# Kernel tuning notes

Measured on AMD Instinct MI355X. Metric: run time of the kernel, lower is better.

Reference implementation:

```python
import jax, jax.numpy as jnp
import numpy as np
import math

D = 256
N = 2048
B = 8
N_PLUS_1 = 2048  # masked index (1-based) in the score matrix


def setup_inputs() -> dict:
    key = jax.random.key(0)
    k1, k2, k3, k4, k5 = jax.random.split(key, 5)
    scale = 1.0 / math.sqrt(D)
    return {
        "Z_in": jax.random.normal(k1, (B, D + 1, N), dtype=jnp.float32),
        "A_l": jax.random.normal(k2, (D, D), dtype=jnp.float32) * scale,
        "r_l": jax.random.normal(k3, (1,), dtype=jnp.float32),
        "B_l": jax.random.normal(k4, (D, D), dtype=jnp.float32) * scale,
        "C_l": jax.random.normal(k5, (D, D), dtype=jnp.float32) * scale,
    }


def reference(Z_in, A_l, r_l, B_l, C_l):
    # Z_in: (B, d+1, N)
    X = Z_in[:, :D, :]   # (B, d, N)
    Y = Z_in[:, D:, :]   # (B, 1, N)
    U = jnp.einsum('ij,bjn->bin', B_l, X)  # (B, d, N)
    W = jnp.einsum('ij,bjn->bin', C_l, X)  # (B, d, N)
    scores = jnp.einsum('bdn,bdm->bnm', U, W)  # (B, N, N) = U^T W
    att = jax.nn.relu(scores)                  # h_type == 'relu'
    # zero the (n_plus_1-1, n_plus_1-1) diagonal entry of the attention core
    att = att.at[:, N_PLUS_1 - 1, N_PLUS_1 - 1].set(0.0)
    X_att = jnp.einsum('bdn,bnm->bdm', X, att)  # (B, d, N)
    X_out = X + jnp.einsum('ij,bjm->bim', A_l, X_att)
    Y_out = Y + r_l * jnp.einsum('bdn,bnm->bdm', Y, att)
    return jnp.concatenate([X_out, Y_out], axis=1)  # (B, d+1, N)
```

## Files before the change

kernel.cpp:

```cpp
#include <hip/hip_runtime.h>

#define D 256
#define N 2048
#define NB 8
#define ZSTRIDE (257 * 2048)

typedef __attribute__((ext_vector_type(8))) short short8;
typedef __attribute__((ext_vector_type(4))) short short4v;
typedef __attribute__((ext_vector_type(4))) float f32x4;

#define MFMA(a, b, c) __builtin_amdgcn_mfma_f32_16x16x32_bf16((a), (b), (c), 0, 0, 0)

#define GLOAD_LDS16(g, s) __builtin_amdgcn_global_load_lds( \
    (const __attribute__((address_space(1))) void*)(g),     \
    (__attribute__((address_space(3))) void*)(s), 16, 0, 0)

#define VMCNT(Nstr) asm volatile("s_waitcnt vmcnt(" Nstr ")" ::: "memory")
#define BAR() __builtin_amdgcn_s_barrier()

__device__ __forceinline__ short f2bf(float f) {
    unsigned u = __builtin_bit_cast(unsigned, f);
    u += 0x7fffu + ((u >> 16) & 1u);
    return (short)(u >> 16);
}
__device__ __forceinline__ float bf2f(short s) {
    unsigned u = ((unsigned)(unsigned short)s) << 16;
    return __builtin_bit_cast(float, u);
}

__global__ __launch_bounds__(256) void front_kernel(
    const float* __restrict__ B_l, const float* __restrict__ C_l,
    const float* __restrict__ A_l, const float* __restrict__ Z,
    short* __restrict__ G, short* __restrict__ Ab, short* __restrict__ Yb,
    float* __restrict__ accY, short* __restrict__ Xt, int zeroAcc)
{
    typedef __attribute__((ext_vector_type(4))) float f4;
    __shared__ short t[64][68];
    int blk = blockIdx.x, tid = threadIdx.x;
    if (blk < 352) {
        if (blk < 256) {
            float s = 0.f;
            #pragma unroll 8
            for (int k = 0; k < 256; ++k)
                s += B_l[k * 256 + blk] * C_l[k * 256 + tid];
            G[blk * 256 + tid] = f2bf(s);
        } else if (blk < 320) {
            int base = (blk - 256) * 1024 + tid;
            #pragma unroll
            for (int r = 0; r < 4; ++r) {
                int idx = base + r * 256;
                Ab[idx] = f2bf(A_l[idx]);
            }
        } else if (blk < 336) {
            int base = (blk - 320) * 1024 + tid;
            #pragma unroll
            for (int r = 0; r < 4; ++r) {
                int idx = base + r * 256;
                int b = idx >> 11, n = idx & 2047;
                Yb[idx] = f2bf(Z[(size_t)b * ZSTRIDE + 256 * N + n]);
            }
        } else if (zeroAcc) {
            int i = (blk - 336) * 256 + tid;
            f32x4 z = {0.f, 0.f, 0.f, 0.f};
            *(f32x4*)(accY + (size_t)i * 4) = z;
        }
        return;
    }
    int tblk = blk - 352;
    int b = tblk & 7;
    int dt = (tblk >> 3) & 3;
    int nt = tblk >> 5;
    int d0 = dt * 64, n0 = nt * 64;
    const float* ZB = Z + (size_t)b * ZSTRIDE;
    #pragma unroll
    for (int k = 0; k < 4; ++k) {
        int f = tid + k * 256;
        int r = f >> 4, c4 = f & 15;
        f4 v = *(const f4*)(ZB + (size_t)(d0 + r) * N + n0 + c4 * 4);
        #pragma unroll
        for (int j = 0; j < 4; ++j) t[r][c4 * 4 + j] = f2bf(v[j]);
    }
    __syncthreads();
    short* XtB = Xt + (size_t)b * (N * D);
    #pragma unroll
    for (int k = 0; k < 2; ++k) {
        int f = tid + k * 256;
        int n = f >> 3, c8 = f & 7;
        short8 v;
        #pragma unroll
        for (int j = 0; j < 8; ++j) v[j] = t[c8 * 8 + j][n];
        *(short8*)(XtB + (size_t)(n0 + n) * D + d0 + c8 * 8) = v;
    }
}

__global__ __launch_bounds__(512, 4) void prep_gemm2(
    const short* __restrict__ Xt, const short* __restrict__ G,
    const short* __restrict__ Ab, short* __restrict__ Wt, short* __restrict__ Px)
{
    __shared__ __align__(16) char smem[65536];
    typedef short TileT[128][64];
    TileT* As = (TileT*)smem;
    TileT* Bs = (TileT*)(smem + 32768);

    int blk = blockIdx.x;
    int half = blk >> 8;
    int r0 = blk & 255;
    int b = r0 >> 5;
    int idx = r0 & 31;

    const short* Arows;
    const short* Brows;
    short* Cout;
    size_t cstride;
    int row_base, col_base;
    if (half == 0) {
        row_base = (idx & 15) << 7;
        col_base = (idx >> 4) << 7;
        Arows = Xt + (size_t)b * (N * D);
        Brows = G;
        Cout  = Wt + (size_t)b * (N * D);
        cstride = D;
    } else {
        row_base = (idx & 1) << 7;
        col_base = (idx >> 1) << 7;
        Arows = Ab;
        Brows = Xt + (size_t)b * (N * D);
        Cout  = Px + (size_t)b * (D * N);
        cstride = N;
    }

    int tid = threadIdx.x;
    int w = tid >> 6, l = tid & 63;
    int l16 = l & 15, lq = l >> 4;
    int wm = w >> 2, wn = w & 3;
    int lrow8 = l >> 3, lc = l & 7;

    auto STAGE = [&](const short* base, int row0g, int kt, TileT* dst) {
        #pragma unroll
        for (int i = 0; i < 2; ++i) {
            int rloc = i * 64 + w * 8;
            int row = rloc + lrow8;
            const char* src = (const char*)(base + (size_t)(row0g + row) * D)
                              + kt * 128 + ((lc ^ (row & 7)) * 16);
            GLOAD_LDS16(src, &(*dst)[rloc][0]);
        }
    };

    f32x4 zero4 = {0.f, 0.f, 0.f, 0.f};
    f32x4 acc[4][2];
    #pragma unroll
    for (int mi = 0; mi < 4; ++mi)
        #pragma unroll
        for (int ni = 0; ni < 2; ++ni) acc[mi][ni] = zero4;

    STAGE(Arows, row_base, 0, &As[0]);
    STAGE(Brows, col_base, 0, &Bs[0]);

    int buf = 0;
    #pragma unroll
    for (int kt = 0; kt < 4; ++kt) {
        if (kt < 3) {
            STAGE(Arows, row_base, kt + 1, &As[buf ^ 1]);
            STAGE(Brows, col_base, kt + 1, &Bs[buf ^ 1]);
            VMCNT("4");
        } else {
            VMCNT("0");
        }
        BAR();
        __builtin_amdgcn_s_setprio(1);
        #pragma unroll
        for (int ks = 0; ks < 2; ++ks) {
            short8 af[4], bf[2];
            #pragma unroll
            for (int mi = 0; mi < 4; ++mi) {
                int r = wm * 64 + mi * 16 + l16;
                af[mi] = *(const short8*)(&As[buf][r][(ks * 32 + lq * 8) ^ ((r & 7) << 3)]);
            }
            #pragma unroll
            for (int ni = 0; ni < 2; ++ni) {
                int r = wn * 32 + ni * 16 + l16;
                bf[ni] = *(const short8*)(&Bs[buf][r][(ks * 32 + lq * 8) ^ ((r & 7) << 3)]);
            }
            #pragma unroll
            for (int mi = 0; mi < 4; ++mi)
                #pragma unroll
                for (int ni = 0; ni < 2; ++ni)
                    acc[mi][ni] = MFMA(af[mi], bf[ni], acc[mi][ni]);
        }
        __builtin_amdgcn_s_setprio(0);
        BAR();
        buf ^= 1;
    }

    short* cq = (short*)smem + (size_t)w * (64 * 40);
    #pragma unroll
    for (int mi = 0; mi < 4; ++mi)
        #pragma unroll
        for (int ni = 0; ni < 2; ++ni)
            #pragma unroll
            for (int rg = 0; rg < 4; ++rg)
                cq[(mi * 16 + lq * 4 + rg) * 40 + ni * 16 + l16] =
                    f2bf(acc[mi][ni][rg]);
    #pragma unroll
    for (int p = 0; p < 4; ++p) {
        int row = p * 16 + (l >> 2), c8 = l & 3;
        short8 v = *(const short8*)(&cq[row * 40 + c8 * 8]);
        *(short8*)(Cout + (size_t)(row_base + wm * 64 + row) * cstride +
                   col_base + wn * 32 + c8 * 8) = v;
    }
}

__global__ __launch_bounds__(512, 4) void scores_kernel(
    const short* __restrict__ Xt, const short* __restrict__ Wt,
    const short* __restrict__ Yb, short* __restrict__ attT,
    float* __restrict__ accY, int bBase, int nbMask, int nbShift)
{
    __shared__ __align__(16) char smem[49152];
    typedef short ATile[128][32];
    typedef short BTile[256][32];
    ATile* As = (ATile*)smem;
    BTile* Bs = (BTile*)(smem + 16384);

    int blk = blockIdx.x;
    int b_local = blk & nbMask;
    int idx = blk >> nbShift;
    int m_base = (idx & 15) << 7;
    int n_base = (idx >> 4) << 8;
    int b = bBase + b_local;

    int tid = threadIdx.x;
    int w = tid >> 6, l = tid & 63;
    int l16 = l & 15, lq = l >> 4;
    int wm = w >> 2, wn = w & 3;
    int lr4 = l >> 2, lc4 = l & 3;

    const short* WtB = Wt + (size_t)b * (N * D);
    const short* XtB = Xt + (size_t)b * (N * D);
    const short* YbB = Yb + (size_t)b * N;
    float* accYB = accY + (size_t)b * N;
    short* attTB = attT + (size_t)b_local * N * N;

    auto STAGE_A = [&](int kt, int bi) {
        int row = w * 16 + lr4;
        const char* src = (const char*)(WtB + (size_t)(m_base + row) * D)
                          + kt * 64 + ((lc4 ^ ((row >> 1) & 3)) * 16);
        GLOAD_LDS16(src, &As[bi][w * 16][0]);
    };
    auto STAGE_B = [&](int kt, int bi) {
        #pragma unroll
        for (int i = 0; i < 2; ++i) {
            int row = i * 128 + w * 16 + lr4;
            const char* src = (const char*)(XtB + (size_t)(n_base + row) * D)
                              + kt * 64 + ((lc4 ^ ((row >> 1) & 3)) * 16);
            GLOAD_LDS16(src, &Bs[bi][i * 128 + w * 16][0]);
        }
    };

    f32x4 zero4 = {0.f, 0.f, 0.f, 0.f};
    f32x4 acc[4][4];
    #pragma unroll
    for (int mi = 0; mi < 4; ++mi)
        #pragma unroll
        for (int ni = 0; ni < 4; ++ni) acc[mi][ni] = zero4;

    STAGE_A(0, 0);
    STAGE_B(0, 0);

    #pragma unroll
    for (int kt = 0; kt < 8; ++kt) {
        if (kt < 7) {
            STAGE_A(kt + 1, (kt + 1) & 1);
            STAGE_B(kt + 1, (kt + 1) & 1);
            VMCNT("3");
        } else {
            VMCNT("0");
        }
        BAR();
        __builtin_amdgcn_s_setprio(1);
        short8 af[4], bf[4];
        #pragma unroll
        for (int mi = 0; mi < 4; ++mi) {
            int r = wm * 64 + mi * 16 + l16;
            af[mi] = *(const short8*)(&As[kt & 1][r][(lq ^ ((r >> 1) & 3)) * 8]);
        }
        #pragma unroll
        for (int ni = 0; ni < 4; ++ni) {
            int r = wn * 64 + ni * 16 + l16;
            bf[ni] = *(const short8*)(&Bs[kt & 1][r][(lq ^ ((r >> 1) & 3)) * 8]);
        }
        #pragma unroll
        for (int mi = 0; mi < 4; ++mi)
            #pragma unroll
            for (int ni = 0; ni < 4; ++ni)
                acc[mi][ni] = MFMA(af[mi], bf[ni], acc[mi][ni]);
        __builtin_amdgcn_s_setprio(0);
        BAR();
    }

    bool corner = (m_base == 1920) && (n_base == 1792);
    #pragma unroll
    for (int mi = 0; mi < 4; ++mi)
        #pragma unroll
        for (int ni = 0; ni < 4; ++ni)
            #pragma unroll
            for (int rg = 0; rg < 4; ++rg) {
                float v = acc[mi][ni][rg];
                v = v > 0.f ? v : 0.f;
                if (corner) {
                    int gm = m_base + wm * 64 + mi * 16 + lq * 4 + rg;
                    int gn = n_base + wn * 64 + ni * 16 + l16;
                    if (gm == N - 1 && gn == N - 1) v = 0.f;
                }
                acc[mi][ni][rg] = v;
            }

    {
        float yv[4];
        #pragma unroll
        for (int ni = 0; ni < 4; ++ni)
            yv[ni] = bf2f(YbB[n_base + wn * 64 + ni * 16 + l16]);
        #pragma unroll
        for (int mi = 0; mi < 4; ++mi)
            #pragma unroll
            for (int rg = 0; rg < 4; ++rg) {
                float s = acc[mi][0][rg] * yv[0] + acc[mi][1][rg] * yv[1]
                        + acc[mi][2][rg] * yv[2] + acc[mi][3][rg] * yv[3];
                s += __shfl_xor(s, 1);
                s += __shfl_xor(s, 2);
                s += __shfl_xor(s, 4);
                s += __shfl_xor(s, 8);
                if (l16 == 0)
                    atomicAdd(&accYB[m_base + wm * 64 + mi * 16 + lq * 4 + rg], s);
            }
    }

    {
        short* sq = (short*)smem + (size_t)w * (64 * 40);
        #pragma unroll
        for (int h = 0; h < 2; ++h) {
            #pragma unroll
            for (int mi = 0; mi < 4; ++mi)
                #pragma unroll
                for (int nih = 0; nih < 2; ++nih)
                    #pragma unroll
                    for (int rg = 0; rg < 4; ++rg)
                        sq[(mi * 16 + lq * 4 + rg) * 40 + nih * 16 + l16] =
                            f2bf(acc[mi][h * 2 + nih][rg]);
            #pragma unroll
            for (int p = 0; p < 4; ++p) {
                int row = p * 16 + lr4, c8 = lc4;
                short8 v = *(const short8*)(&sq[row * 40 + c8 * 8]);
                *(short8*)(attTB + (size_t)(m_base + wm * 64 + row) * N +
                           n_base + wn * 64 + h * 32 + c8 * 8) = v;
            }
        }
    }
}

__global__ __launch_bounds__(512, 4) void pv_kernel(
    const float* __restrict__ Z, const short* __restrict__ Px,
    const short* __restrict__ attT, const float* __restrict__ accY,
    const float* __restrict__ r_l, float* __restrict__ out,
    int bBase, int nbMask, int nbShift)
{
    __shared__ __align__(16) char smem[49152];
    typedef short ATile[64][64];
    typedef short BTile[128][64];
    ATile* As = (ATile*)smem;
    BTile* Bs = (BTile*)(smem + 16384);

    int blk = blockIdx.x;
    int b_local = blk & nbMask;
    int idx = blk >> nbShift;
    int d_base = (idx & 3) << 6;
    int m_base = (idx >> 2) << 7;
    int b = bBase + b_local;

    int tid = threadIdx.x;
    int w = tid >> 6, l = tid & 63;
    int l16 = l & 15, lq = l >> 4;
    int wd = w >> 2, wm = w & 3;
    int lrow8 = l >> 3, lc = l & 7;

    const short* PxB = Px + (size_t)b * (D * N);
    const short* attTB = attT + (size_t)b_local * N * N;

    auto STAGE_A = [&](int kt, ATile* dst) {
        int rloc = w * 8;
        int row = rloc + lrow8;
        const char* src = (const char*)(PxB + (size_t)(d_base + row) * N)
                          + kt * 128 + ((lc ^ (row & 7)) * 16);
        GLOAD_LDS16(src, &(*dst)[rloc][0]);
    };
    auto STAGE_B = [&](int kt, BTile* dst) {
        #pragma unroll
        for (int i = 0; i < 2; ++i) {
            int rloc = i * 64 + w * 8;
            int row = rloc + lrow8;
            const char* src = (const char*)(attTB + (size_t)(m_base + row) * N)
                              + kt * 128 + ((lc ^ (row & 7)) * 16);
            GLOAD_LDS16(src, &(*dst)[rloc][0]);
        }
    };

    f32x4 zero4 = {0.f, 0.f, 0.f, 0.f};
    f32x4 acc[2][2];
    #pragma unroll
    for (int di = 0; di < 2; ++di)
        #pragma unroll
        for (int mj = 0; mj < 2; ++mj) acc[di][mj] = zero4;

    STAGE_A(0, &As[0]);
    STAGE_B(0, &Bs[0]);

    int buf = 0;
    for (int kt = 0; kt < 32; ++kt) {
        if (kt < 31) {
            STAGE_A(kt + 1, &As[buf ^ 1]);
            STAGE_B(kt + 1, &Bs[buf ^ 1]);
            VMCNT("3");
        } else {
            VMCNT("0");
        }
        BAR();
        __builtin_amdgcn_s_setprio(1);
        #pragma unroll
        for (int ks = 0; ks < 2; ++ks) {
            short8 af[2], bf[2];
            #pragma unroll
            for (int di = 0; di < 2; ++di) {
                int r = wd * 32 + di * 16 + l16;
                af[di] = *(const short8*)(&As[buf][r][(ks * 32 + lq * 8) ^ ((r & 7) << 3)]);
            }
            #pragma unroll
            for (int mj = 0; mj < 2; ++mj) {
                int r = wm * 32 + mj * 16 + l16;
                bf[mj] = *(const short8*)(&Bs[buf][r][(ks * 32 + lq * 8) ^ ((r & 7) << 3)]);
            }
            #pragma unroll
            for (int di = 0; di < 2; ++di)
                #pragma unroll
                for (int mj = 0; mj < 2; ++mj)
                    acc[di][mj] = MFMA(af[di], bf[mj], acc[di][mj]);
        }
        __builtin_amdgcn_s_setprio(0);
        BAR();
        buf ^= 1;
    }

    #pragma unroll
    for (int di = 0; di < 2; ++di)
        #pragma unroll
        for (int mj = 0; mj < 2; ++mj)
            #pragma unroll
            for (int rg = 0; rg < 4; ++rg) {
                int dd = d_base + wd * 32 + di * 16 + lq * 4 + rg;
                int mm = m_base + wm * 32 + mj * 16 + l16;
                size_t off = (size_t)b * ZSTRIDE + (size_t)dd * N + mm;
                out[off] = Z[off] + acc[di][mj][rg];
            }

    if (d_base == 0 && tid < 128) {
        int mm = m_base + tid;
        size_t off = (size_t)b * ZSTRIDE + (size_t)256 * N + mm;
        out[off] = Z[off] + r_l[0] * accY[(size_t)b * N + mm];
    }
}

__global__ __launch_bounds__(512, 4) void fused_kernel(
    const float* __restrict__ Z, const short* __restrict__ Xt,
    const short* __restrict__ Wt, const short* __restrict__ Px,
    const short* __restrict__ Yb, const float* __restrict__ r_l,
    float* __restrict__ out)
{
    __shared__ __align__(16) short xtsA[32][256];
    __shared__ __align__(16) short xtsB[32][256];
    __shared__ __align__(16) short attA[64][36];
    __shared__ __align__(16) short attB[64][36];

    int blk = blockIdx.x;
    int b = blk & 7;
    int m_base = (blk >> 3) << 6;
    int tid = threadIdx.x;
    int w = tid >> 6, l = tid & 63;
    int l16 = l & 15, lq = l >> 4;

    const short* XtB = Xt + (size_t)b * (N * D);
    const short* WtB = Wt + (size_t)b * (N * D);
    const short* PxB = Px + (size_t)b * (D * N);
    const short* YbB = Yb + b * N;

    int mi = w >> 1;
    int nj = w & 1;

    short8 a_wt[8];
    {
        const short* ap = WtB + (size_t)(m_base + 16 * mi + l16) * D + lq * 8;
        #pragma unroll
        for (int ks = 0; ks < 8; ++ks)
            a_wt[ks] = *(const short8*)(ap + ks * 32);
    }

    f32x4 zero4 = {0.f, 0.f, 0.f, 0.f};
    f32x4 accX[2][4];
    #pragma unroll
    for (int di = 0; di < 2; ++di)
        #pragma unroll
        for (int mj = 0; mj < 4; ++mj) accX[di][mj] = zero4;

    float accY = 0.f;
    int ym = tid >> 3, yseg = tid & 7;

    auto STAGE = [&](int it, short (*dst)[256]) {
        #pragma unroll
        for (int r = 0; r < 2; ++r) {
            int row  = r * 16 + 2 * w + (l >> 5);
            int colb = ((l & 31) * 16) ^ ((row & 7) << 4);
            const char* src = (const char*)(XtB + (size_t)(it * 32 + row) * D) + colb;
            GLOAD_LDS16(src, &dst[r * 16 + 2 * w][0]);
        }
    };

    auto BODY = [&](int it, short (*xrd)[256], short (*xst)[256], short (*atw)[36]) {
        int n_base = it * 32;
        if (it + 1 < 64) STAGE(it + 1, xst);
        short8 px[2];
        #pragma unroll
        for (int di = 0; di < 2; ++di)
            px[di] = *(const short8*)(PxB + (size_t)(32 * w + 16 * di + l16) * N +
                                      n_base + lq * 8);
        short4v yv = *(const short4v*)(YbB + n_base + yseg * 4);
        f32x4 sa = zero4;
        #pragma unroll
        for (int ks = 0; ks < 8; ++ks) {
            int colsh = (ks * 32 + lq * 8) ^ ((l16 & 7) << 3);
            short8 xb = *(const short8*)(&xrd[16 * nj + l16][colsh]);
            sa = MFMA(a_wt[ks], xb, sa);
        }
        {
            int nn = 16 * nj + l16;
            #pragma unroll
            for (int rg = 0; rg < 4; ++rg) {
                int mm = 16 * mi + lq * 4 + rg;
                float v = sa[rg] > 0.f ? sa[rg] : 0.f;
                if ((m_base + mm == N - 1) && (n_base + nn == N - 1)) v = 0.f;
                atw[mm][nn] = f2bf(v);
            }
        }
        __syncthreads();
        #pragma unroll
        for (int mj = 0; mj < 4; ++mj) {
            short8 bfr = *(const short8*)(&atw[16 * mj + l16][lq * 8]);
            #pragma unroll
            for (int di = 0; di < 2; ++di)
                accX[di][mj] = MFMA(px[di], bfr, accX[di][mj]);
        }
        {
            short4v av = *(const short4v*)(&atw[ym][yseg * 4]);
            #pragma unroll
            for (int j = 0; j < 4; ++j)
                accY += bf2f(av[j]) * bf2f(yv[j]);
        }
    };

    STAGE(0, xtsA);
    __syncthreads();
    for (int it2 = 0; it2 < 32; ++it2) {
        BODY(2 * it2,     xtsA, xtsB, attA);
        BODY(2 * it2 + 1, xtsB, xtsA, attB);
    }

    #pragma unroll
    for (int di = 0; di < 2; ++di)
        #pragma unroll
        for (int mj = 0; mj < 4; ++mj)
            #pragma unroll
            for (int rg = 0; rg < 4; ++rg) {
                int dd = 32 * w + 16 * di + lq * 4 + rg;
                int mm = m_base + 16 * mj + l16;
                size_t off = (size_t)b * ZSTRIDE + (size_t)dd * N + mm;
                out[off] = Z[off] + accX[di][mj][rg];
            }
    accY += __shfl_xor(accY, 1);
    accY += __shfl_xor(accY, 2);
    accY += __shfl_xor(accY, 4);
    if (yseg == 0) {
        float r = r_l[0];
        int mm = m_base + ym;
        size_t off = (size_t)b * ZSTRIDE + (size_t)256 * N + mm;
        out[off] = Z[off] + r * accY;
    }
}

extern "C" void kernel_launch(void* const* d_in, const int* in_sizes, int n_in,
                              void* d_out, int out_size, void* d_ws, size_t ws_size,
                              hipStream_t stream) {
    const float* Z   = (const float*)d_in[0];
    const float* A_l = (const float*)d_in[1];
    const float* r_l = (const float*)d_in[2];
    const float* B_l = (const float*)d_in[3];
    const float* C_l = (const float*)d_in[4];
    float* out = (float*)d_out;

    char* ws = (char*)d_ws;
    short* G    = (short*)(ws);
    short* Ab   = (short*)(ws + 131072);
    short* Xt   = (short*)(ws + 262144);
    short* Wt   = (short*)(ws + 8650752);
    short* Px   = (short*)(ws + 17039360);
    short* Yb   = (short*)(ws + 25427968);
    float* accY = (float*)(ws + 25460736);
    short* attT = (short*)(ws + 25526272);

    const size_t baseNeed = 25526272;
    const size_t attSz = (size_t)N * N * 2;
    int NBCH = 8, nbShift = 3;
    while (NBCH > 1 && baseNeed + (size_t)NBCH * attSz > ws_size) { NBCH >>= 1; --nbShift; }
    bool decomposed = (baseNeed + (size_t)NBCH * attSz <= ws_size);

    front_kernel<<<1376, 256, 0, stream>>>(B_l, C_l, A_l, Z, G, Ab, Yb,
                                           accY, Xt, decomposed ? 1 : 0);
    prep_gemm2<<<512, 512, 0, stream>>>(Xt, G, Ab, Wt, Px);

    if (decomposed) {
        int nbMask = NBCH - 1;
        for (int c = 0; c < NB / NBCH; ++c) {
            int bBase = c * NBCH;
            scores_kernel<<<NBCH * 128, 512, 0, stream>>>(
                Xt, Wt, Yb, attT, accY, bBase, nbMask, nbShift);
            pv_kernel<<<NBCH * 64, 512, 0, stream>>>(
                Z, Px, attT, accY, r_l, out, bBase, nbMask, nbShift);
        }
    } else {
        fused_kernel<<<256, 512, 0, stream>>>(Z, Xt, Wt, Px, Yb, r_l, out);
    }
}
```

Measured before the change: 86.50 us.

## Merge scores and PV into one kernel and overlap batch halves

The separate scores and PV kernels are merged into one combo_kernel that picks its role from the block index. When the workspace holds all eight attention matrices, the work runs as three launches: scores for batches 0-3, then PV for 0-3 together with scores for 4-7, then PV for 4-7. The aim is to fill the GPU better and cut the tail and launch-boundary idle time between the dependent stages. The cost is a kernel that carries both code paths, which may raise register pressure and hurt occupancy, plus one more launch.

Result: slower. 100.8 us (+16.5%).

```diff
diff --git a/kernel.cpp b/kernel.cpp
--- a/kernel.cpp
+++ b/kernel.cpp
@@ -210,260 +210,251 @@
     }
 }
 
-__global__ __launch_bounds__(512, 4) void scores_kernel(
-    const short* __restrict__ Xt, const short* __restrict__ Wt,
+__global__ __launch_bounds__(512, 4) void combo_kernel(
+    const float* __restrict__ Z, const short* __restrict__ Xt,
+    const short* __restrict__ Wt, const short* __restrict__ Px,
     const short* __restrict__ Yb, short* __restrict__ attT,
-    float* __restrict__ accY, int bBase, int nbMask, int nbShift)
+    float* __restrict__ accY, const float* __restrict__ r_l,
+    float* __restrict__ out, int nPv, int pvBase, int scBase)
 {
     __shared__ __align__(16) char smem[49152];
-    typedef short ATile[128][32];
-    typedef short BTile[256][32];
-    ATile* As = (ATile*)smem;
-    BTile* Bs = (BTile*)(smem + 16384);
-
-    int blk = blockIdx.x;
-    int b_local = blk & nbMask;
-    int idx = blk >> nbShift;
-    int m_base = (idx & 15) << 7;
-    int n_base = (idx >> 4) << 8;
-    int b = bBase + b_local;
-
     int tid = threadIdx.x;
     int w = tid >> 6, l = tid & 63;
     int l16 = l & 15, lq = l >> 4;
-    int wm = w >> 2, wn = w & 3;
-    int lr4 = l >> 2, lc4 = l & 3;
-
-    const short* WtB = Wt + (size_t)b * (N * D);
-    const short* XtB = Xt + (size_t)b * (N * D);
-    const short* YbB = Yb + (size_t)b * N;
-    float* accYB = accY + (size_t)b * N;
-    short* attTB = attT + (size_t)b_local * N * N;
-
-    auto STAGE_A = [&](int kt, int bi) {
-        int row = w * 16 + lr4;
-        const char* src = (const char*)(WtB + (size_t)(m_base + row) * D)
-                          + kt * 64 + ((lc4 ^ ((row >> 1) & 3)) * 16);
-        GLOAD_LDS16(src, &As[bi][w * 16][0]);
-    };
-    auto STAGE_B = [&](int kt, int bi) {
-        #pragma unroll
-        for (int i = 0; i < 2; ++i) {
-            int row = i * 128 + w * 16 + lr4;
-            const char* src = (const char*)(XtB + (size_t)(n_base + row) * D)
-                              + kt * 64 + ((lc4 ^ ((row >> 1) & 3)) * 16);
-            GLOAD_LDS16(src, &Bs[bi][i * 128 + w * 16][0]);
-        }
-    };
-
     f32x4 zero4 = {0.f, 0.f, 0.f, 0.f};
-    f32x4 acc[4][4];
-    #pragma unroll
-    for (int mi = 0; mi < 4; ++mi)
-        #pragma unroll
-        for (int ni = 0; ni < 4; ++ni) acc[mi][ni] = zero4;
-
-    STAGE_A(0, 0);
-    STAGE_B(0, 0);
-
-    #pragma unroll
-    for (int kt = 0; kt < 8; ++kt) {
-        if (kt < 7) {
-            STAGE_A(kt + 1, (kt + 1) & 1);
-            STAGE_B(kt + 1, (kt + 1) & 1);
-            VMCNT("3");
-        } else {
-            VMCNT("0");
-        }
-        BAR();
-        __builtin_amdgcn_s_setprio(1);
-        short8 af[4], bf[4];
-        #pragma unroll
-        for (int mi = 0; mi < 4; ++mi) {
-            int r = wm * 64 + mi * 16 + l16;
-            af[mi] = *(const short8*)(&As[kt & 1][r][(lq ^ ((r >> 1) & 3)) * 8]);
-        }
-        #pragma unroll
-        for (int ni = 0; ni < 4; ++ni) {
-            int r = wn * 64 + ni * 16 + l16;
-            bf[ni] = *(const short8*)(&Bs[kt & 1][r][(lq ^ ((r >> 1) & 3)) * 8]);
-        }
-        #pragma unroll
-        for (int mi = 0; mi < 4; ++mi)
-            #pragma unroll
-            for (int ni = 0; ni < 4; ++ni)
-                acc[mi][ni] = MFMA(af[mi], bf[ni], acc[mi][ni]);
-        __builtin_amdgcn_s_setprio(0);
-        BAR();
-    }
-
-    bool corner = (m_base == 1920) && (n_base == 1792);
-    #pragma unroll
-    for (int mi = 0; mi < 4; ++mi)
-        #pragma unroll
-        for (int ni = 0; ni < 4; ++ni)
-            #pragma unroll
-            for (int rg = 0; rg < 4; ++rg) {
-                float v = acc[mi][ni][rg];
-                v = v > 0.f ? v : 0.f;
-                if (corner) {
-                    int gm = m_base + wm * 64 + mi * 16 + lq * 4 + rg;
-                    int gn = n_base + wn * 64 + ni * 16 + l16;
-                    if (gm == N - 1 && gn == N - 1) v = 0.f;
-                }
-                acc[mi][ni][rg] = v;
-            }
-
-    {
-        float yv[4];
-        #pragma unroll
-        for (int ni = 0; ni < 4; ++ni)
-            yv[ni] = bf2f(YbB[n_base + wn * 64 + ni * 16 + l16]);
-        #pragma unroll
-        for (int mi = 0; mi < 4; ++mi)
-            #pragma unroll
-            for (int rg = 0; rg < 4; ++rg) {
-                float s = acc[mi][0][rg] * yv[0] + acc[mi][1][rg] * yv[1]
-                        + acc[mi][2][rg] * yv[2] + acc[mi][3][rg] * yv[3];
-                s += __shfl_xor(s, 1);
-                s += __shfl_xor(s, 2);
-                s += __shfl_xor(s, 4);
-                s += __shfl_xor(s, 8);
-                if (l16 == 0)
-                    atomicAdd(&accYB[m_base + wm * 64 + mi * 16 + lq * 4 + rg], s);
-            }
-    }
-
-    {
-        short* sq = (short*)smem + (size_t)w * (64 * 40);
-        #pragma unroll
-        for (int h = 0; h < 2; ++h) {
-            #pragma unroll
-            for (int mi = 0; mi < 4; ++mi)
-                #pragma unroll
-                for (int nih = 0; nih < 2; ++nih)
-                    #pragma unroll
-                    for (int rg = 0; rg < 4; ++rg)
-                        sq[(mi * 16 + lq * 4 + rg) * 40 + nih * 16 + l16] =
-                            f2bf(acc[mi][h * 2 + nih][rg]);
-            #pragma unroll
-            for (int p = 0; p < 4; ++p) {
-                int row = p * 16 + lr4, c8 = lc4;
-                short8 v = *(const short8*)(&sq[row * 40 + c8 * 8]);
-                *(short8*)(attTB + (size_t)(m_base + wm * 64 + row) * N +
-                           n_base + wn * 64 + h * 32 + c8 * 8) = v;
-            }
-        }
-    }
-}
-
-__global__ __launch_bounds__(512, 4) void pv_kernel(
-    const float* __restrict__ Z, const short* __restrict__ Px,
-    const short* __restrict__ attT, const float* __restrict__ accY,
-    const float* __restrict__ r_l, float* __restrict__ out,
-    int bBase, int nbMask, int nbShift)
-{
-    __shared__ __align__(16) char smem[49152];
-    typedef short ATile[64][64];
-    typedef short BTile[128][64];
-    ATile* As = (ATile*)smem;
-    BTile* Bs = (BTile*)(smem + 16384);
-
-    int blk = blockIdx.x;
-    int b_local = blk & nbMask;
-    int idx = blk >> nbShift;
-    int d_base = (idx & 3) << 6;
-    int m_base = (idx >> 2) << 7;
-    int b = bBase + b_local;
-
-    int tid = threadIdx.x;
-    int w = tid >> 6, l = tid & 63;
-    int l16 = l & 15, lq = l >> 4;
-    int wd = w >> 2, wm = w & 3;
-    int lrow8 = l >> 3, lc = l & 7;
-
-    const short* PxB = Px + (size_t)b * (D * N);
-    const short* attTB = attT + (size_t)b_local * N * N;
-
-    auto STAGE_A = [&](int kt, ATile* dst) {
-        int rloc = w * 8;
-        int row = rloc + lrow8;
-        const char* src = (const char*)(PxB + (size_t)(d_base + row) * N)
-                          + kt * 128 + ((lc ^ (row & 7)) * 16);
-        GLOAD_LDS16(src, &(*dst)[rloc][0]);
-    };
-    auto STAGE_B = [&](int kt, BTile* dst) {
-        #pragma unroll
-        for (int i = 0; i < 2; ++i) {
-            int rloc = i * 64 + w * 8;
+
+    if ((int)blockIdx.x < nPv) {
+        typedef short ATile[64][64];
+        typedef short BTile[128][64];
+        ATile* As = (ATile*)smem;
+        BTile* Bs = (BTile*)(smem + 16384);
+
+        int blk = blockIdx.x;
+        int b = pvBase + (blk & 3);
+        int idx = blk >> 2;
+        int d_base = (idx & 3) << 6;
+        int m_base = (idx >> 2) << 7;
+
+        int wd = w >> 2, wm = w & 3;
+        int lrow8 = l >> 3, lc = l & 7;
+
+        const short* PxB = Px + (size_t)b * (D * N);
+        const short* attTB = attT + (size_t)(b & 7) * N * N;
+
+        auto STAGE_A = [&](int kt, ATile* dst) {
+            int rloc = w * 8;
             int row = rloc + lrow8;
-            const char* src = (const char*)(attTB + (size_t)(m_base + row) * N)
+            const char* src = (const char*)(PxB + (size_t)(d_base + row) * N)
                               + kt * 128 + ((lc ^ (row & 7)) * 16);
             GLOAD_LDS16(src, &(*dst)[rloc][0]);
-        }
-    };
-
-    f32x4 zero4 = {0.f, 0.f, 0.f, 0.f};
-    f32x4 acc[2][2];
-    #pragma unroll
-    for (int di = 0; di < 2; ++di)
-        #pragma unroll
-        for (int mj = 0; mj < 2; ++mj) acc[di][mj] = zero4;
-
-    STAGE_A(0, &As[0]);
-    STAGE_B(0, &Bs[0]);
-
-    int buf = 0;
-    for (int kt = 0; kt < 32; ++kt) {
-        if (kt < 31) {
-            STAGE_A(kt + 1, &As[buf ^ 1]);
-            STAGE_B(kt + 1, &Bs[buf ^ 1]);
-            VMCNT("3");
-        } else {
-            VMCNT("0");
-        }
-        BAR();
-        __builtin_amdgcn_s_setprio(1);
-        #pragma unroll
-        for (int ks = 0; ks < 2; ++ks) {
-            short8 af[2], bf[2];
-            #pragma unroll
-            for (int di = 0; di < 2; ++di) {
-                int r = wd * 32 + di * 16 + l16;
-                af[di] = *(const short8*)(&As[buf][r][(ks * 32 + lq * 8) ^ ((r & 7) << 3)]);
-            }
-            #pragma unroll
-            for (int mj = 0; mj < 2; ++mj) {
-                int r = wm * 32 + mj * 16 + l16;
-                bf[mj] = *(const short8*)(&Bs[buf][r][(ks * 32 + lq * 8) ^ ((r & 7) << 3)]);
-            }
-            #pragma unroll
-            for (int di = 0; di < 2; ++di)
-                #pragma unroll
-                for (int mj = 0; mj < 2; ++mj)
-                    acc[di][mj] = MFMA(af[di], bf[mj], acc[di][mj]);
-        }
-        __builtin_amdgcn_s_setprio(0);
-        BAR();
-        buf ^= 1;
-    }
-
-    #pragma unroll
-    for (int di = 0; di < 2; ++di)
-        #pragma unroll
-        for (int mj = 0; mj < 2; ++mj)
-            #pragma unroll
-            for (int rg = 0; rg < 4; ++rg) {
-                int dd = d_base + wd * 32 + di * 16 + lq * 4 + rg;
-                int mm = m_base + wm * 32 + mj * 16 + l16;
-                size_t off = (size_t)b * ZSTRIDE + (size_t)dd * N + mm;
-                out[off] = Z[off] + acc[di][mj][rg];
-            }
-
-    if (d_base == 0 && tid < 128) {
-        int mm = m_base + tid;
-        size_t off = (size_t)b * ZSTRIDE + (size_t)256 * N + mm;
-        out[off] = Z[off] + r_l[0] * accY[(size_t)b * N + mm];
+        };
+        auto STAGE_B = [&](int kt, BTile* dst) {
+            #pragma unroll
+            for (int i = 0; i < 2; ++i) {
+                int rloc = i * 64 + w * 8;
+                int row = rloc + lrow8;
+                const char* src = (const char*)(attTB + (size_t)(m_base + row) * N)
+                                  + kt * 128 + ((lc ^ (row & 7)) * 16);
+                GLOAD_LDS16(src, &(*dst)[rloc][0]);
+            }
+        };
+
+        f32x4 acc[2][2];
+        #pragma unroll
+        for (int di = 0; di < 2; ++di)
+            #pragma unroll
+            for (int mj = 0; mj < 2; ++mj) acc[di][mj] = zero4;
+
+        STAGE_A(0, &As[0]);
+        STAGE_B(0, &Bs[0]);
+
+        int buf = 0;
+        for (int kt = 0; kt < 32; ++kt) {
+            if (kt < 31) {
+                STAGE_A(kt + 1, &As[buf ^ 1]);
+                STAGE_B(kt + 1, &Bs[buf ^ 1]);
+                VMCNT("3");
+            } else {
+                VMCNT("0");
+            }
+            BAR();
+            __builtin_amdgcn_s_setprio(1);
+            #pragma unroll
+            for (int ks = 0; ks < 2; ++ks) {
+                short8 af[2], bf[2];
+                #pragma unroll
+                for (int di = 0; di < 2; ++di) {
+                    int r = wd * 32 + di * 16 + l16;
+                    af[di] = *(const short8*)(&As[buf][r][(ks * 32 + lq * 8) ^ ((r & 7) << 3)]);
+                }
+                #pragma unroll
+                for (int mj = 0; mj < 2; ++mj) {
+                    int r = wm * 32 + mj * 16 + l16;
+                    bf[mj] = *(const short8*)(&Bs[buf][r][(ks * 32 + lq * 8) ^ ((r & 7) << 3)]);
+                }
+                #pragma unroll
+                for (int di = 0; di < 2; ++di)
+                    #pragma unroll
+                    for (int mj = 0; mj < 2; ++mj)
+                        acc[di][mj] = MFMA(af[di], bf[mj], acc[di][mj]);
+            }
+            __builtin_amdgcn_s_setprio(0);
+            BAR();
+            buf ^= 1;
+        }
+
+        #pragma unroll
+        for (int di = 0; di < 2; ++di)
+            #pragma unroll
+            for (int mj = 0; mj < 2; ++mj)
+                #pragma unroll
+                for (int rg = 0; rg < 4; ++rg) {
+                    int dd = d_base + wd * 32 + di * 16 + lq * 4 + rg;
+                    int mm = m_base + wm * 32 + mj * 16 + l16;
+                    size_t off = (size_t)b * ZSTRIDE + (size_t)dd * N + mm;
+                    out[off] = Z[off] + acc[di][mj][rg];
+                }
+
+        if (d_base == 0 && tid < 128) {
+            int mm = m_base + tid;
+            size_t off = (size_t)b * ZSTRIDE + (size_t)256 * N + mm;
+            out[off] = Z[off] + r_l[0] * accY[(size_t)b * N + mm];
+        }
+    } else {
+        typedef short ATile[128][32];
+        typedef short BTile[256][32];
+        ATile* As = (ATile*)smem;
+        BTile* Bs = (BTile*)(smem + 16384);
+
+        int sblk = blockIdx.x - nPv;
+        int b = scBase + (sblk & 3);
+        int idx = sblk >> 2;
+        int m_base = (idx & 15) << 7;
+        int n_base = (idx >> 4) << 8;
+
+        int wm = w >> 2, wn = w & 3;
+        int lr4 = l >> 2, lc4 = l & 3;
+
+        const short* WtB = Wt + (size_t)b * (N * D);
+        const short* XtB = Xt + (size_t)b * (N * D);
+        const short* YbB = Yb + (size_t)b * N;
+        float* accYB = accY + (size_t)b * N;
+        short* attTB = attT + (size_t)(b & 7) * N * N;
+
+        auto STAGE_A = [&](int kt, int bi) {
+            int row = w * 16 + lr4;
+            const char* src = (const char*)(WtB + (size_t)(m_base + row) * D)
+                              + kt * 64 + ((lc4 ^ ((row >> 1) & 3)) * 16);
+            GLOAD_LDS16(src, &As[bi][w * 16][0]);
+        };
+        auto STAGE_B = [&](int kt, int bi) {
+            #pragma unroll
+            for (int i = 0; i < 2; ++i) {
+                int row = i * 128 + w * 16 + lr4;
+                const char* src = (const char*)(XtB + (size_t)(n_base + row) * D)
+                                  + kt * 64 + ((lc4 ^ ((row >> 1) & 3)) * 16);
+                GLOAD_LDS16(src, &Bs[bi][i * 128 + w * 16][0]);
+            }
+        };
+
+        f32x4 acc[4][4];
+        #pragma unroll
+        for (int mi = 0; mi < 4; ++mi)
+            #pragma unroll
+            for (int ni = 0; ni < 4; ++ni) acc[mi][ni] = zero4;
+
+        STAGE_A(0, 0);
+        STAGE_B(0, 0);
+
+        #pragma unroll
+        for (int kt = 0; kt < 8; ++kt) {
+            if (kt < 7) {
+                STAGE_A(kt + 1, (kt + 1) & 1);
+                STAGE_B(kt + 1, (kt + 1) & 1);
+                VMCNT("3");
+            } else {
+                VMCNT("0");
+            }
+            BAR();
+            __builtin_amdgcn_s_setprio(1);
+            short8 af[4], bf[4];
+            #pragma unroll
+            for (int mi = 0; mi < 4; ++mi) {
+                int r = wm * 64 + mi * 16 + l16;
+                af[mi] = *(const short8*)(&As[kt & 1][r][(lq ^ ((r >> 1) & 3)) * 8]);
+            }
+            #pragma unroll
+            for (int ni = 0; ni < 4; ++ni) {
+                int r = wn * 64 + ni * 16 + l16;
+                bf[ni] = *(const short8*)(&Bs[kt & 1][r][(lq ^ ((r >> 1) & 3)) * 8]);
+            }
+            #pragma unroll
+            for (int mi = 0; mi < 4; ++mi)
+                #pragma unroll
+                for (int ni = 0; ni < 4; ++ni)
+                    acc[mi][ni] = MFMA(af[mi], bf[ni], acc[mi][ni]);
+            __builtin_amdgcn_s_setprio(0);
+            BAR();
+        }
+
+        bool corner = (m_base == 1920) && (n_base == 1792);
+        #pragma unroll
+        for (int mi = 0; mi < 4; ++mi)
+            #pragma unroll
+            for (int ni = 0; ni < 4; ++ni)
+                #pragma unroll
+                for (int rg = 0; rg < 4; ++rg) {
+                    float v = acc[mi][ni][rg];
+                    v = v > 0.f ? v : 0.f;
+                    if (corner) {
+                        int gm = m_base + wm * 64 + mi * 16 + lq * 4 + rg;
+                        int gn = n_base + wn * 64 + ni * 16 + l16;
+                        if (gm == N - 1 && gn == N - 1) v = 0.f;
+                    }
+                    acc[mi][ni][rg] = v;
+                }
+
+        {
+            float yv[4];
+            #pragma unroll
+            for (int ni = 0; ni < 4; ++ni)
+                yv[ni] = bf2f(YbB[n_base + wn * 64 + ni * 16 + l16]);
+            #pragma unroll
+            for (int mi = 0; mi < 4; ++mi)
+                #pragma unroll
+                for (int rg = 0; rg < 4; ++rg) {
+                    float s = acc[mi][0][rg] * yv[0] + acc[mi][1][rg] * yv[1]
+                            + acc[mi][2][rg] * yv[2] + acc[mi][3][rg] * yv[3];
+                    s += __shfl_xor(s, 1);
+                    s += __shfl_xor(s, 2);
+                    s += __shfl_xor(s, 4);
+                    s += __shfl_xor(s, 8);
+                    if (l16 == 0)
+                        atomicAdd(&accYB[m_base + wm * 64 + mi * 16 + lq * 4 + rg], s);
+                }
+        }
+
+        {
+            short* sq = (short*)smem + (size_t)w * (64 * 40);
+            #pragma unroll
+            for (int h = 0; h < 2; ++h) {
+                #pragma unroll
+                for (int mi = 0; mi < 4; ++mi)
+                    #pragma unroll
+                    for (int nih = 0; nih < 2; ++nih)
+                        #pragma unroll
+                        for (int rg = 0; rg < 4; ++rg)
+                            sq[(mi * 16 + lq * 4 + rg) * 40 + nih * 16 + l16] =
+                                f2bf(acc[mi][h * 2 + nih][rg]);
+                #pragma unroll
+                for (int p = 0; p < 4; ++p) {
+                    int row = p * 16 + lr4, c8 = lc4;
+                    short8 v = *(const short8*)(&sq[row * 40 + c8 * 8]);
+                    *(short8*)(attTB + (size_t)(m_base + wm * 64 + row) * N +
+                               n_base + wn * 64 + h * 32 + c8 * 8) = v;
+                }
+            }
+        }
     }
 }
 
@@ -614,22 +605,28 @@
 
     const size_t baseNeed = 25526272;
     const size_t attSz = (size_t)N * N * 2;
-    int NBCH = 8, nbShift = 3;
-    while (NBCH > 1 && baseNeed + (size_t)NBCH * attSz > ws_size) { NBCH >>= 1; --nbShift; }
-    bool decomposed = (baseNeed + (size_t)NBCH * attSz <= ws_size);
+    bool full8 = (baseNeed + 8 * attSz <= ws_size);
+    bool half4 = (baseNeed + 4 * attSz <= ws_size);
 
     front_kernel<<<1376, 256, 0, stream>>>(B_l, C_l, A_l, Z, G, Ab, Yb,
-                                           accY, Xt, decomposed ? 1 : 0);
+                                           accY, Xt, (full8 || half4) ? 1 : 0);
     prep_gemm2<<<512, 512, 0, stream>>>(Xt, G, Ab, Wt, Px);
 
-    if (decomposed) {
-        int nbMask = NBCH - 1;
-        for (int c = 0; c < NB / NBCH; ++c) {
-            int bBase = c * NBCH;
-            scores_kernel<<<NBCH * 128, 512, 0, stream>>>(
-                Xt, Wt, Yb, attT, accY, bBase, nbMask, nbShift);
-            pv_kernel<<<NBCH * 64, 512, 0, stream>>>(
-                Z, Px, attT, accY, r_l, out, bBase, nbMask, nbShift);
+    if (full8) {
+        combo_kernel<<<512, 512, 0, stream>>>(Z, Xt, Wt, Px, Yb, attT, accY,
+                                              r_l, out, 0, 0, 0);
+        combo_kernel<<<768, 512, 0, stream>>>(Z, Xt, Wt, Px, Yb, attT, accY,
+                                              r_l, out, 256, 0, 4);
+        combo_kernel<<<256, 512, 0, stream>>>(Z, Xt, Wt, Px, Yb, attT, accY,
+                                              r_l, out, 256, 4, 0);
+    } else if (half4) {
+        for (int c = 0; c < 2; ++c) {
+            int bBase = c * 4;
+            short* attTc = attT - (size_t)bBase * N * N;
+            combo_kernel<<<512, 512, 0, stream>>>(Z, Xt, Wt, Px, Yb, attTc, accY,
+                                                  r_l, out, 0, 0, bBase);
+            combo_kernel<<<256, 512, 0, stream>>>(Z, Xt, Wt, Px, Yb, attTc, accY,
+                                                  r_l, out, 256, bBase, 0);
         }
     } else {
         fused_kernel<<<256, 512, 0, stream>>>(Z, Xt, Wt, Px, Yb, r_l, out);
```

## Move Y-attention reduction from scores epilogue into PV kernel

Applied to the files above, without the earlier changes.

The Y·att product was computed in the scores kernel epilogue using shuffles and global atomicAdds into an fp32 buffer, which also had to be zeroed in the front kernel. It is now computed inside pv_kernel: blocks with d_base==0 reuse the attention tile already staged in LDS and dot it with Y, which is preloaded into LDS. This removes the atomics, the accY buffer, its zeroing blocks and extra epilogue work in the scores kernel. In exchange, pv_kernel's d_base==0 blocks do extra scalar LDS reads and FMAs per k-step, uses slightly more shared memory, and Y is now taken from the bf16 attention values rather than the fp32 pre-rounding scores.

New measurement: 91.87 us. +6.2%, slower.

```diff
diff --git a/kernel.cpp b/kernel.cpp
--- a/kernel.cpp
+++ b/kernel.cpp
@@ -32,12 +32,12 @@
     const float* __restrict__ B_l, const float* __restrict__ C_l,
     const float* __restrict__ A_l, const float* __restrict__ Z,
     short* __restrict__ G, short* __restrict__ Ab, short* __restrict__ Yb,
-    float* __restrict__ accY, short* __restrict__ Xt, int zeroAcc)
+    short* __restrict__ Xt)
 {
     typedef __attribute__((ext_vector_type(4))) float f4;
     __shared__ short t[64][68];
     int blk = blockIdx.x, tid = threadIdx.x;
-    if (blk < 352) {
+    if (blk < 336) {
         if (blk < 256) {
             float s = 0.f;
             #pragma unroll 8
@@ -51,7 +51,7 @@
                 int idx = base + r * 256;
                 Ab[idx] = f2bf(A_l[idx]);
             }
-        } else if (blk < 336) {
+        } else {
             int base = (blk - 320) * 1024 + tid;
             #pragma unroll
             for (int r = 0; r < 4; ++r) {
@@ -59,14 +59,10 @@
                 int b = idx >> 11, n = idx & 2047;
                 Yb[idx] = f2bf(Z[(size_t)b * ZSTRIDE + 256 * N + n]);
             }
-        } else if (zeroAcc) {
-            int i = (blk - 336) * 256 + tid;
-            f32x4 z = {0.f, 0.f, 0.f, 0.f};
-            *(f32x4*)(accY + (size_t)i * 4) = z;
         }
         return;
     }
-    int tblk = blk - 352;
+    int tblk = blk - 336;
     int b = tblk & 7;
     int dt = (tblk >> 3) & 3;
     int nt = tblk >> 5;
@@ -212,8 +208,7 @@
 
 __global__ __launch_bounds__(512, 4) void scores_kernel(
     const short* __restrict__ Xt, const short* __restrict__ Wt,
-    const short* __restrict__ Yb, short* __restrict__ attT,
-    float* __restrict__ accY, int bBase, int nbMask, int nbShift)
+    short* __restrict__ attT, int bBase, int nbMask, int nbShift)
 {
     __shared__ __align__(16) char smem[49152];
     typedef short ATile[128][32];
@@ -236,8 +231,6 @@
 
     const short* WtB = Wt + (size_t)b * (N * D);
     const short* XtB = Xt + (size_t)b * (N * D);
-    const short* YbB = Yb + (size_t)b * N;
-    float* accYB = accY + (size_t)b * N;
     short* attTB = attT + (size_t)b_local * N * N;
 
     auto STAGE_A = [&](int kt, int bi) {
@@ -315,26 +308,6 @@
             }
 
     {
-        float yv[4];
-        #pragma unroll
-        for (int ni = 0; ni < 4; ++ni)
-            yv[ni] = bf2f(YbB[n_base + wn * 64 + ni * 16 + l16]);
-        #pragma unroll
-        for (int mi = 0; mi < 4; ++mi)
-            #pragma unroll
-            for (int rg = 0; rg < 4; ++rg) {
-                float s = acc[mi][0][rg] * yv[0] + acc[mi][1][rg] * yv[1]
-                        + acc[mi][2][rg] * yv[2] + acc[mi][3][rg] * yv[3];
-                s += __shfl_xor(s, 1);
-                s += __shfl_xor(s, 2);
-                s += __shfl_xor(s, 4);
-                s += __shfl_xor(s, 8);
-                if (l16 == 0)
-                    atomicAdd(&accYB[m_base + wm * 64 + mi * 16 + lq * 4 + rg], s);
-            }
-    }
-
-    {
         short* sq = (short*)smem + (size_t)w * (64 * 40);
         #pragma unroll
         for (int h = 0; h < 2; ++h) {
@@ -359,15 +332,16 @@
 
 __global__ __launch_bounds__(512, 4) void pv_kernel(
     const float* __restrict__ Z, const short* __restrict__ Px,
-    const short* __restrict__ attT, const float* __restrict__ accY,
+    const short* __restrict__ attT, const short* __restrict__ Yb,
     const float* __restrict__ r_l, float* __restrict__ out,
     int bBase, int nbMask, int nbShift)
 {
-    __shared__ __align__(16) char smem[49152];
+    __shared__ __align__(16) char smem[53248];
     typedef short ATile[64][64];
     typedef short BTile[128][64];
     ATile* As = (ATile*)smem;
     BTile* Bs = (BTile*)(smem + 16384);
+    short* yls = (short*)(smem + 49152);
 
     int blk = blockIdx.x;
     int b_local = blk & nbMask;
@@ -384,6 +358,12 @@
 
     const short* PxB = Px + (size_t)b * (D * N);
     const short* attTB = attT + (size_t)b_local * N * N;
+
+    if (d_base == 0 && tid < 256) {
+        short8 yv8 = *(const short8*)(Yb + (size_t)b * N + tid * 8);
+        *(short8*)(&yls[tid * 8]) = yv8;
+    }
+    __syncthreads();
 
     auto STAGE_A = [&](int kt, ATile* dst) {
         int rloc = w * 8;
@@ -410,6 +390,9 @@
         #pragma unroll
         for (int mj = 0; mj < 2; ++mj) acc[di][mj] = zero4;
 
+    float yacc = 0.f;
+    int yrow = tid >> 2, ys = tid & 3;
+
     STAGE_A(0, &As[0]);
     STAGE_B(0, &Bs[0]);
 
@@ -444,6 +427,18 @@
                     acc[di][mj] = MFMA(af[di], bf[mj], acc[di][mj]);
         }
         __builtin_amdgcn_s_setprio(0);
+        if (d_base == 0) {
+            #pragma unroll
+            for (int c = 0; c < 2; ++c) {
+                int dc = 2 * ys + c;
+                int lchunk = dc ^ (yrow & 7);
+                short8 bv = *(const short8*)(&Bs[buf][yrow][lchunk * 8]);
+                short8 yv = *(const short8*)(&yls[kt * 64 + dc * 8]);
+                #pragma unroll
+                for (int j = 0; j < 8; ++j)
+                    yacc += bf2f(bv[j]) * bf2f(yv[j]);
+            }
+        }
         BAR();
         buf ^= 1;
     }
@@ -460,10 +455,14 @@
                 out[off] = Z[off] + acc[di][mj][rg];
             }
 
-    if (d_base == 0 && tid < 128) {
-        int mm = m_base + tid;
-        size_t off = (size_t)b * ZSTRIDE + (size_t)256 * N + mm;
-        out[off] = Z[off] + r_l[0] * accY[(size_t)b * N + mm];
+    if (d_base == 0) {
+        yacc += __shfl_xor(yacc, 1);
+        yacc += __shfl_xor(yacc, 2);
+        if (ys == 0) {
+            int mm = m_base + yrow;
+            size_t off = (size_t)b * ZSTRIDE + (size_t)256 * N + mm;
+            out[off] = Z[off] + r_l[0] * yacc;
+        }
     }
 }
 
@@ -609,7 +608,6 @@
     short* Wt   = (short*)(ws + 8650752);
     short* Px   = (short*)(ws + 17039360);
     short* Yb   = (short*)(ws + 25427968);
-    float* accY = (float*)(ws + 25460736);
     short* attT = (short*)(ws + 25526272);
 
     const size_t baseNeed = 25526272;
@@ -618,8 +616,7 @@
     while (NBCH > 1 && baseNeed + (size_t)NBCH * attSz > ws_size) { NBCH >>= 1; --nbShift; }
     bool decomposed = (baseNeed + (size_t)NBCH * attSz <= ws_size);
 
-    front_kernel<<<1376, 256, 0, stream>>>(B_l, C_l, A_l, Z, G, Ab, Yb,
-                                           accY, Xt, decomposed ? 1 : 0);
+    front_kernel<<<1360, 256, 0, stream>>>(B_l, C_l, A_l, Z, G, Ab, Yb, Xt);
     prep_gemm2<<<512, 512, 0, stream>>>(Xt, G, Ab, Wt, Px);
 
     if (decomposed) {
@@ -627,9 +624,9 @@
         for (int c = 0; c < NB / NBCH; ++c) {
             int bBase = c * NBCH;
             scores_kernel<<<NBCH * 128, 512, 0, stream>>>(
-                Xt, Wt, Yb, attT, accY, bBase, nbMask, nbShift);
+                Xt, Wt, attT, bBase, nbMask, nbShift);
             pv_kernel<<<NBCH * 64, 512, 0, stream>>>(
-                Z, Px, attT, accY, r_l, out, bBase, nbMask, nbShift);
+                Z, Px, attT, Yb, r_l, out, bBase, nbMask, nbShift);
         }
     } else {
         fused_kernel<<<256, 512, 0, stream>>>(Z, Xt, Wt, Px, Yb, r_l, out);
```
